# Kernel tuning notes

Hardware: AMD Instinct MI355X
Metric: run time of the kernel (lower is better)

The kernel has to match this reference:

```python
import jax, jax.numpy as jnp
import numpy as np

LN_EPS = 1e-5

def _ln(x, g, b):
    m = x.mean(-1, keepdims=True)
    v = ((x - m) ** 2).mean(-1, keepdims=True)
    return (x - m) * jax.lax.rsqrt(v + LN_EPS) * g + b

def setup_inputs() -> dict:
    key = jax.random.key(0)
    B, Q, K, H, NH, L = 4, 32, 8192, 1024, 16, 128
    ks = jax.random.split(key, 10)
    def p(k, shape):
        return jax.random.normal(k, shape, jnp.float32) * 0.02
    return {
        "question_emb": jax.random.normal(ks[0], (B, Q, H), jnp.float32),
        "context_emb": jax.random.normal(ks[1], (B, K, H), jnp.float32),
        "Wq_l": p(ks[2], (H, H)), "bq_l": jnp.zeros((H,), jnp.float32),
        "Wk_l": p(ks[3], (H, H)), "bk_l": jnp.zeros((H,), jnp.float32),
        "Wq_g": p(ks[4], (H, H)), "bq_g": jnp.zeros((H,), jnp.float32),
        "Wk_g": p(ks[5], (H, H)), "bk_g": jnp.zeros((H,), jnp.float32),
        "ln_g": jnp.ones((H,), jnp.float32), "ln_b": jnp.zeros((H,), jnp.float32),
        "gp_W1": p(ks[6], (2 * H, H)), "gp_b1": jnp.zeros((H,), jnp.float32),
        "gp_W2": p(ks[7], (H, 1)), "gp_b2": jnp.zeros((1,), jnp.float32),
        "num_heads": NH,
        "chunk_len": L,
    }

def reference(question_emb, context_emb, Wq_l, bq_l, Wk_l, bk_l,
              Wq_g, bq_g, Wk_g, bk_g, ln_g, ln_b,
              gp_W1, gp_b1, gp_W2, gp_b2, num_heads, chunk_len):
    B, Qn, H = question_emb.shape
    K = context_emb.shape[1]
    nh, L = num_heads, chunk_len
    d = H // nh
    J = K // L
    scale = 1.0 / np.sqrt(d)

    # ---- Global scorer: one cross-attn over all K, then per-chunk mean pooling ----
    qh = (question_emb @ Wq_g + bq_g).reshape(B, Qn, nh, d).transpose(0, 2, 1, 3)   # [B,nh,Q,d]
    kh = (context_emb @ Wk_g + bk_g).reshape(B, K, nh, d).transpose(0, 2, 1, 3)     # [B,nh,K,d]
    wg = jax.nn.softmax(jnp.einsum('bhqd,bhkd->bhqk', qh, kh) * scale, axis=-1)     # [B,nh,Q,K]
    attn = wg.mean(axis=(1, 2))                                                     # [B,K]
    global_scores = jax.nn.softmax(attn.reshape(B, J, L).mean(-1), axis=-1)         # [B,J]

    # ---- Local scorer: per-chunk cross-attn (batched over chunks), max-over-keys pooling ----
    qh_l = (question_emb @ Wq_l + bq_l).reshape(B, Qn, nh, d).transpose(0, 2, 1, 3)  # [B,nh,Q,d]
    kh_l = (context_emb @ Wk_l + bk_l).reshape(B, J, L, nh, d).transpose(0, 1, 3, 2, 4)  # [B,J,nh,L,d]
    s_l = jnp.einsum('bhqd,bjhld->bjhql', qh_l, kh_l) * scale                        # [B,J,nh,Q,L]
    w_l = jax.nn.softmax(s_l, axis=-1)
    local_scores = jax.nn.softmax(w_l.max(-1).mean(axis=(2, 3)), axis=-1)            # [B,J]

    # ---- Router: LN'd mean-pool vecs -> gate MLP -> fuse -> softmax ----
    q_vec = _ln(question_emb.mean(1), ln_g, ln_b)                                    # [B,H]
    c_vec = _ln(context_emb.reshape(B, J, L, H).mean(2), ln_g, ln_b)                 # [B,J,H]
    g_in = jnp.concatenate([jnp.broadcast_to(q_vec[:, None, :], (B, J, H)), c_vec], -1)
    h1 = jax.nn.gelu(g_in @ gp_W1 + gp_b1, approximate=False)
    gate = jax.nn.sigmoid(h1 @ gp_W2 + gp_b2)[..., 0]                                # [B,J]
    fused = gate * local_scores + (1.0 - gate) * global_scores
    final_scores = jax.nn.softmax(fused, axis=-1)                                    # [B,J]
    global_gate = final_scores.mean(-1).reshape(B, 1, 1)
    return final_scores, local_scores, global_scores, global_gate
```

## Files before the change

kernel.cpp:

```cpp
#include <hip/hip_runtime.h>
#include <math.h>

#define B_    4
#define QN    32
#define KN    8192
#define HDIM  1024
#define NHD   16
#define DH    64
#define LCH   128
#define JCH   64

typedef float f32x4 __attribute__((ext_vector_type(4)));
typedef short s16x8 __attribute__((ext_vector_type(8)));
typedef unsigned short u16;

__device__ __forceinline__ u16 f2bf(float f) {
  unsigned u = __float_as_uint(f);
  u += 0x7fffu + ((u >> 16) & 1u);
  return (u16)(u >> 16);
}

__device__ __forceinline__ void llds16(const void* g, void* l) {
  __builtin_amdgcn_global_load_lds((const __attribute__((address_space(1))) unsigned int*)g,
                                   (__attribute__((address_space(3))) unsigned int*)l,
                                   16, 0, 0);
}

__device__ __forceinline__ void gemm64_direct(const float* __restrict__ A, const float* __restrict__ Bm,
                                              float* __restrict__ C, int m0, int n0, char* smem) {
  float (*As)[17] = (float(*)[17])smem;
  float (*Bs)[64] = (float(*)[64])(smem + 4352);
  int t = threadIdx.x;
  int tm = t >> 4, tn = t & 15;
  int ra = t >> 2, ka = (t & 3) * 4;
  int kb = t >> 4, nb = (t & 15) * 4;
  float c[4][4];
#pragma unroll
  for (int i = 0; i < 4; ++i)
#pragma unroll
    for (int j = 0; j < 4; ++j) c[i][j] = 0.f;
  float4 va = *(const float4*)(A + (size_t)(m0 + ra) * HDIM + ka);
  float4 vb = *(const float4*)(Bm + (size_t)kb * HDIM + n0 + nb);
  for (int kk = 0; kk < HDIM; kk += 16) {
    As[ra][ka] = va.x; As[ra][ka + 1] = va.y; As[ra][ka + 2] = va.z; As[ra][ka + 3] = va.w;
    *(float4*)&Bs[kb][nb] = vb;
    __syncthreads();
    if (kk + 16 < HDIM) {
      va = *(const float4*)(A + (size_t)(m0 + ra) * HDIM + kk + 16 + ka);
      vb = *(const float4*)(Bm + (size_t)(kk + 16 + kb) * HDIM + n0 + nb);
    }
#pragma unroll
    for (int kq = 0; kq < 16; ++kq) {
      float a0 = As[tm * 4 + 0][kq], a1 = As[tm * 4 + 1][kq];
      float a2 = As[tm * 4 + 2][kq], a3 = As[tm * 4 + 3][kq];
      float b0 = Bs[kq][tn * 4 + 0], b1 = Bs[kq][tn * 4 + 1];
      float b2 = Bs[kq][tn * 4 + 2], b3 = Bs[kq][tn * 4 + 3];
      c[0][0] += a0 * b0; c[0][1] += a0 * b1; c[0][2] += a0 * b2; c[0][3] += a0 * b3;
      c[1][0] += a1 * b0; c[1][1] += a1 * b1; c[1][2] += a1 * b2; c[1][3] += a1 * b3;
      c[2][0] += a2 * b0; c[2][1] += a2 * b1; c[2][2] += a2 * b2; c[2][3] += a2 * b3;
      c[3][0] += a3 * b0; c[3][1] += a3 * b1; c[3][2] += a3 * b2; c[3][3] += a3 * b3;
    }
    __syncthreads();
  }
#pragma unroll
  for (int i = 0; i < 4; ++i)
#pragma unroll
    for (int j = 0; j < 4; ++j)
      C[(size_t)(m0 + tm * 4 + i) * HDIM + n0 + tn * 4 + j] = c[i][j];
}

__global__ __launch_bounds__(256) void k_cvt(const float* __restrict__ ctx, u16* __restrict__ ctxb,
                                             float* __restrict__ csum4,
                                             const float* __restrict__ question,
                                             const float* __restrict__ Wq_g, const float* __restrict__ Wq_l,
                                             float* __restrict__ qh,
                                             const float* __restrict__ g, const float* __restrict__ lb,
                                             float* __restrict__ qvec, float* __restrict__ qpart) {
  __shared__ __align__(16) char smem[8448];
  int blk = blockIdx.x, t = threadIdx.x;
  if (blk < 64) {
    int s2 = blk >> 5, mt = (blk >> 4) & 1, ntile = blk & 15;
    gemm64_direct(question, s2 ? Wq_l : Wq_g, qh + (size_t)s2 * 131072, mt * 64, ntile * 64, smem);
  } else if (blk < 68) {
    int b = blk - 64;
    const float* p = question + (size_t)b * QN * HDIM + t * 4;
    float a0 = 0, a1 = 0, a2 = 0, a3 = 0;
    for (int r = 0; r < QN; ++r) {
      float4 v = *(const float4*)(p + (size_t)r * HDIM);
      a0 += v.x; a1 += v.y; a2 += v.z; a3 += v.w;
    }
    const float sc = 1.0f / QN;
    a0 *= sc; a1 *= sc; a2 *= sc; a3 *= sc;
    float s = a0 + a1 + a2 + a3;
    float ss = a0 * a0 + a1 * a1 + a2 * a2 + a3 * a3;
#pragma unroll
    for (int o = 1; o < 64; o <<= 1) { s += __shfl_xor(s, o, 64); ss += __shfl_xor(ss, o, 64); }
    float* sm = (float*)smem; float* sq = sm + 4;
    int wid = t >> 6, lane = t & 63;
    if (lane == 0) { sm[wid] = s; sq[wid] = ss; }
    __syncthreads();
    float S = sm[0] + sm[1] + sm[2] + sm[3], SS = sq[0] + sq[1] + sq[2] + sq[3];
    float mu = S / HDIM;
    float inv = rsqrtf(SS / HDIM - mu * mu + 1e-5f);
    int c = t * 4;
    float4 o;
    o.x = (a0 - mu) * inv * g[c + 0] + lb[c + 0];
    o.y = (a1 - mu) * inv * g[c + 1] + lb[c + 1];
    o.z = (a2 - mu) * inv * g[c + 2] + lb[c + 2];
    o.w = (a3 - mu) * inv * g[c + 3] + lb[c + 3];
    *(float4*)&qvec[(size_t)b * HDIM + c] = o;
  } else if (blk == 68) {
    float4 z = make_float4(0.f, 0.f, 0.f, 0.f);
#pragma unroll
    for (int i = 0; i < 4; ++i) ((float4*)qpart)[t * 4 + i] = z;
  } else {
    int cb = blk - 69;
    int bj = cb >> 2, seg = cb & 3;
    const float* p = ctx + ((size_t)bj * LCH + seg * 32) * HDIM + t * 4;
    u16* op = ctxb + ((size_t)bj * LCH + seg * 32) * HDIM + t * 4;
    float a0 = 0, a1 = 0, a2 = 0, a3 = 0;
    for (int r0 = 0; r0 < 32; r0 += 8) {
      float4 v[8];
#pragma unroll
      for (int r = 0; r < 8; ++r) v[r] = *(const float4*)(p + (size_t)(r0 + r) * HDIM);
#pragma unroll
      for (int r = 0; r < 8; ++r) {
        ushort4 o;
        o.x = f2bf(v[r].x); o.y = f2bf(v[r].y); o.z = f2bf(v[r].z); o.w = f2bf(v[r].w);
        *(ushort4*)(op + (size_t)(r0 + r) * HDIM) = o;
        a0 += v[r].x; a1 += v[r].y; a2 += v[r].z; a3 += v[r].w;
      }
    }
    *(float4*)&csum4[((size_t)bj * 4 + seg) * HDIM + t * 4] = make_float4(a0, a1, a2, a3);
  }
}

__global__ __launch_bounds__(256) void k_mid(const float* __restrict__ qh,
                                             const float* __restrict__ Wk_g, const float* __restrict__ Wk_l,
                                             const float* __restrict__ bq_g, const float* __restrict__ bq_l,
                                             u16* __restrict__ Ab,
                                             const float* __restrict__ bk_g, const float* __restrict__ bk_l,
                                             float* __restrict__ sbias,
                                             const float* __restrict__ qvec, const float* __restrict__ W1,
                                             float* __restrict__ qpart,
                                             const float* __restrict__ csum4,
                                             const float* __restrict__ g, const float* __restrict__ lb,
                                             float* __restrict__ cvec) {
  __shared__ __align__(16) char smem[8448];
  int blk = blockIdx.x, t = threadIdx.x;
  if (blk < 512) {
    int ct = blk & 3, slot = (blk >> 2) & 31, b = blk >> 7;
    int s2 = slot >> 4, h = slot & 15;
    const float* qhp = qh + (size_t)(s2 * 4 + b) * QN * HDIM;
    const float* Wk = s2 ? Wk_l : Wk_g;
    const float* bq = s2 ? bq_l : bq_g;
    float (*qs)[DH] = (float(*)[DH])smem;
    {
      int q = t >> 3, doff = (t & 7) * 8;
      const float4* src = (const float4*)(qhp + (size_t)q * HDIM + h * DH + doff);
      float4 b0 = *(const float4*)(bq + h * DH + doff);
      float4 b1 = *(const float4*)(bq + h * DH + doff + 4);
      float4 v0 = src[0], v1 = src[1];
      qs[q][doff + 0] = v0.x + b0.x; qs[q][doff + 1] = v0.y + b0.y;
      qs[q][doff + 2] = v0.z + b0.z; qs[q][doff + 3] = v0.w + b0.w;
      qs[q][doff + 4] = v1.x + b1.x; qs[q][doff + 5] = v1.y + b1.y;
      qs[q][doff + 6] = v1.z + b1.z; qs[q][doff + 7] = v1.w + b1.w;
    }
    __syncthreads();
    int c = ct * 256 + t;
    float w[DH];
    const float* wr = Wk + (size_t)c * HDIM + h * DH;
#pragma unroll
    for (int d = 0; d < DH; d += 4) {
      float4 v = *(const float4*)(wr + d);
      w[d] = v.x; w[d + 1] = v.y; w[d + 2] = v.z; w[d + 3] = v.w;
    }
    u16* outp = Ab + ((size_t)b * HDIM + s2 * 512 + h * QN) * HDIM + c;
    for (int q = 0; q < QN; ++q) {
      float acc = 0.f;
#pragma unroll
      for (int d = 0; d < DH; ++d) acc += qs[q][d] * w[d];
      outp[(size_t)q * HDIM] = f2bf(acc * 0.125f);
    }
  } else if (blk < 768) {
    int id = blk - 512;
    int nt = id & 3, b = (id >> 2) & 3, ks = id >> 4;
    int n = nt * 256 + t;
    const float* qv = qvec + (size_t)b * HDIM + ks * 64;
    const float* wp = W1 + (size_t)ks * 64 * HDIM + n;
    float acc = 0.f;
#pragma unroll 8
    for (int c = 0; c < 64; ++c) acc += qv[c] * wp[(size_t)c * HDIM];
    atomicAdd(&qpart[(size_t)b * HDIM + n], acc);
  } else if (blk < 1024) {
    int bj = blk - 768;
    const float* cs = csum4 + (size_t)bj * 4 * HDIM + t * 4;
    float4 v0 = *(const float4*)(cs);
    float4 v1 = *(const float4*)(cs + HDIM);
    float4 v2 = *(const float4*)(cs + 2 * HDIM);
    float4 v3 = *(const float4*)(cs + 3 * HDIM);
    const float sc = 1.0f / LCH;
    float a0 = (v0.x + v1.x + v2.x + v3.x) * sc;
    float a1 = (v0.y + v1.y + v2.y + v3.y) * sc;
    float a2 = (v0.z + v1.z + v2.z + v3.z) * sc;
    float a3 = (v0.w + v1.w + v2.w + v3.w) * sc;
    float s = a0 + a1 + a2 + a3;
    float ss = a0 * a0 + a1 * a1 + a2 * a2 + a3 * a3;
#pragma unroll
    for (int o = 1; o < 64; o <<= 1) { s += __shfl_xor(s, o, 64); ss += __shfl_xor(ss, o, 64); }
    float* sm = (float*)smem; float* sq = sm + 4;
    int wid = t >> 6, lane = t & 63;
    if (lane == 0) { sm[wid] = s; sq[wid] = ss; }
    __syncthreads();
    float S = sm[0] + sm[1] + sm[2] + sm[3], SS = sq[0] + sq[1] + sq[2] + sq[3];
    float mu = S / HDIM;
    float inv = rsqrtf(SS / HDIM - mu * mu + 1e-5f);
    int c = t * 4;
    float4 o;
    o.x = (a0 - mu) * inv * g[c + 0] + lb[c + 0];
    o.y = (a1 - mu) * inv * g[c + 1] + lb[c + 1];
    o.z = (a2 - mu) * inv * g[c + 2] + lb[c + 2];
    o.w = (a3 - mu) * inv * g[c + 3] + lb[c + 3];
    *(float4*)&cvec[(size_t)bj * HDIM + c] = o;
  } else {
    int i = (blk - 1024) * 256 + t;
    int b = i >> 10, n = i & (HDIM - 1);
    int s2 = n >> 9, hq = n & 511, h = hq >> 5, q = hq & 31;
    const float* qr = qh + ((size_t)(s2 * 4 + b) * QN + q) * HDIM + h * DH;
    const float* bk = (s2 ? bk_l : bk_g) + h * DH;
    const float* bq = (s2 ? bq_l : bq_g) + h * DH;
    float acc = 0.f;
#pragma unroll
    for (int d = 0; d < DH; ++d) acc += (qr[d] + bq[d]) * bk[d];
    sbias[i] = acc * 0.125f;
  }
}

__global__ __launch_bounds__(512, 2) void k_scores(const u16* __restrict__ ctxb, const u16* __restrict__ Ab,
                                                   const float* __restrict__ sbias,
                                                   float* __restrict__ mglob, float* __restrict__ zglob,
                                                   float* __restrict__ locinv) {
  __shared__ u16 lds[65536];
  u16* A0 = lds;           u16* B0 = lds + 16384;
  u16* A1 = lds + 32768;   u16* B1 = lds + 49152;
  int bid = blockIdx.x;
  int work = (bid & 7) * 64 + (bid >> 3);
  int b = work >> 7, rem = work & 127, rt = rem >> 2, nt = rem & 3;
  int t = threadIdx.x, wid = t >> 6, lane = t & 63;
  int wm = wid >> 2, wn = wid & 3;
  int lrow = lane & 15, lkg = lane >> 4;

  const u16* ctx0 = ctxb + ((size_t)b * KN + rt * 256) * HDIM;
  const u16* Afp  = Ab + ((size_t)b * HDIM + nt * 256) * HDIM;

  int grow = wid * 8 + (lane >> 3);
  int gslot = (lane & 7) ^ (lane >> 3);
  const u16* gA[4]; const u16* gB[4]; int dof[4];
#pragma unroll
  for (int s = 0; s < 4; ++s) {
    gA[s] = ctx0 + (size_t)(s * 64 + grow) * HDIM + gslot * 8;
    gB[s] = Afp + (size_t)(s * 64 + grow) * HDIM + gslot * 8;
    dof[s] = s * 4096 + wid * 512;
  }

  int rowA = (wm * 128 + lrow) * 64;
  int rowB = (wn * 64 + lrow) * 64;
  int p8[2];
#pragma unroll
  for (int ks = 0; ks < 2; ++ks) p8[ks] = ((ks * 4 + lkg) ^ (lane & 7)) * 8;

  f32x4 acc[8][4];
#pragma unroll
  for (int mi = 0; mi < 8; ++mi)
#pragma unroll
    for (int ni = 0; ni < 4; ++ni) acc[mi][ni] = 0.f;

#define STAGE(AT, BT, KT) { \
  _Pragma("unroll") for (int s = 0; s < 4; ++s) { \
    llds16(gA[s] + (KT) * 64, (AT) + dof[s]); \
    llds16(gB[s] + (KT) * 64, (BT) + dof[s]); } }

#define COMPUTE(AT, BT) { \
  _Pragma("unroll") for (int ks = 0; ks < 2; ++ks) { \
    const u16* pA = (AT) + rowA + p8[ks]; \
    const u16* pB = (BT) + rowB + p8[ks]; \
    s16x8 av[8], bv[4]; \
    _Pragma("unroll") for (int mi = 0; mi < 8; ++mi) av[mi] = *(const s16x8*)(pA + mi * 1024); \
    _Pragma("unroll") for (int ni = 0; ni < 4; ++ni) bv[ni] = *(const s16x8*)(pB + ni * 1024); \
    _Pragma("unroll") for (int mi = 0; mi < 8; ++mi) \
    _Pragma("unroll") for (int ni = 0; ni < 4; ++ni) \
      acc[mi][ni] = __builtin_amdgcn_mfma_f32_16x16x32_bf16(av[mi], bv[ni], acc[mi][ni], 0, 0, 0); } }

#define SYNCN(N) { asm volatile("s_waitcnt vmcnt(" #N ")" ::: "memory"); \
                   __builtin_amdgcn_s_barrier(); \
                   __builtin_amdgcn_sched_barrier(0); }

#define SUB(KT, CA, CB, SA, SB, FULL) { \
  if (FULL) { STAGE(SA, SB, (KT) + 1); } \
  if (FULL) { SYNCN(8) } else { SYNCN(0) } \
  __builtin_amdgcn_s_setprio(1); \
  COMPUTE(CA, CB); \
  __builtin_amdgcn_s_setprio(0); \
  __builtin_amdgcn_s_barrier(); }

  STAGE(A0, B0, 0);
  SUB(0,  A0, B0, A1, B1, 1)
  SUB(1,  A1, B1, A0, B0, 1)
  SUB(2,  A0, B0, A1, B1, 1)
  SUB(3,  A1, B1, A0, B0, 1)
  SUB(4,  A0, B0, A1, B1, 1)
  SUB(5,  A1, B1, A0, B0, 1)
  SUB(6,  A0, B0, A1, B1, 1)
  SUB(7,  A1, B1, A0, B0, 1)
  SUB(8,  A0, B0, A1, B1, 1)
  SUB(9,  A1, B1, A0, B0, 1)
  SUB(10, A0, B0, A1, B1, 1)
  SUB(11, A1, B1, A0, B0, 1)
  SUB(12, A0, B0, A1, B1, 1)
  SUB(13, A1, B1, A0, B0, 1)
  SUB(14, A0, B0, A1, B1, 1)
  SUB(15, A1, B1, A0, B0, 0)
#undef STAGE
#undef COMPUTE
#undef SYNCN
#undef SUB

  int jc = rt * 2 + wm;
  float sb[4];
#pragma unroll
  for (int ni = 0; ni < 4; ++ni)
    sb[ni] = sbias[b * HDIM + nt * 256 + wn * 64 + ni * 16 + lrow];
#pragma unroll
  for (int ni = 0; ni < 4; ++ni) {
    float m = -1e30f;
#pragma unroll
    for (int mi = 0; mi < 8; ++mi)
#pragma unroll
      for (int r = 0; r < 4; ++r) m = fmaxf(m, acc[mi][ni][r]);
    m += sb[ni];
    m = fmaxf(m, __shfl_xor(m, 16, 64));
    m = fmaxf(m, __shfl_xor(m, 32, 64));
    float z = 0.f;
#pragma unroll
    for (int mi = 0; mi < 8; ++mi)
#pragma unroll
      for (int r = 0; r < 4; ++r) z += __expf(acc[mi][ni][r] + sb[ni] - m);
    z += __shfl_xor(z, 16, 64);
    z += __shfl_xor(z, 32, 64);
    if (lane < 16) {
      int n = nt * 256 + wn * 64 + ni * 16 + lane;
      if (n < 512) {
        size_t o = ((size_t)b * 512 + n) * JCH + jc;
        mglob[o] = m; zglob[o] = z;
      } else {
        locinv[((size_t)b * JCH + jc) * 512 + (n - 512)] = 1.0f / z;
      }
    }
  }
}

__global__ __launch_bounds__(256) void k_post(const float* __restrict__ cvec, const float* __restrict__ W1,
                                              float* __restrict__ h1,
                                              const float* __restrict__ mglob, const float* __restrict__ zglob,
                                              float* __restrict__ Mh, float* __restrict__ Zr) {
  __shared__ __align__(16) char smem[8448];
  int blk = blockIdx.x, t = threadIdx.x;
  if (blk < 64) {
    int mt = blk >> 4, ntile = blk & 15;
    gemm64_direct(cvec, W1 + 1048576, h1, mt * 64, ntile * 64, smem);
  } else {
    int id = (blk - 64) * 256 + t;
    int b = id >> 9, hq = id & 511;
    const float* mg = mglob + ((size_t)b * 512 + hq) * JCH;
    const float* zg = zglob + ((size_t)b * 512 + hq) * JCH;
    float m = -1e30f;
    for (int j = 0; j < JCH; ++j) m = fmaxf(m, mg[j]);
    float z = 0.f;
    for (int j = 0; j < JCH; ++j) z += zg[j] * __expf(mg[j] - m);
    Mh[id] = m;
    Zr[id] = 1.0f / z;
  }
}

__global__ __launch_bounds__(256) void k_chunk(const float* __restrict__ mglob, const float* __restrict__ zglob,
                                               const float* __restrict__ locinv,
                                               const float* __restrict__ Mh, const float* __restrict__ Zr,
                                               const float* __restrict__ h1, const float* __restrict__ qpart,
                                               const float* __restrict__ b1, const float* __restrict__ W2,
                                               float* __restrict__ abuf, float* __restrict__ lbuf,
                                               float* __restrict__ gbuf) {
  int bj = blockIdx.x, t = threadIdx.x;
  int b = bj >> 6, j = bj & 63;
  const float* mg = mglob + (size_t)b * 512 * JCH + j;
  const float* zg = zglob + (size_t)b * 512 * JCH + j;
  const float* lp = locinv + (size_t)bj * 512;
  const float* Mb = Mh + (size_t)b * 512;
  const float* Zb = Zr + (size_t)b * 512;
  float a = 0.f, l = 0.f, gsum = 0.f;
  for (int hq = t; hq < 512; hq += 256) {
    a += zg[(size_t)hq * JCH] * __expf(mg[(size_t)hq * JCH] - Mb[hq]) * Zb[hq];
    l += lp[hq];
  }
  const float* hp = h1 + (size_t)bj * HDIM;
  const float* qp = qpart + (size_t)b * HDIM;
  for (int n = t; n < HDIM; n += 256) {
    float x = hp[n] + qp[n] + b1[n];
    x = x * 0.5f * (1.0f + erff(x * 0.70710678118654752f));
    gsum += x * W2[n];
  }
#pragma unroll
  for (int o = 1; o < 64; o <<= 1) {
    a += __shfl_xor(a, o, 64); l += __shfl_xor(l, o, 64); gsum += __shfl_xor(gsum, o, 64);
  }
  __shared__ float ra[4], rl[4], rg[4];
  int wid = t >> 6, lane = t & 63;
  if (lane == 0) { ra[wid] = a; rl[wid] = l; rg[wid] = gsum; }
  __syncthreads();
  if (t == 0) {
    abuf[bj] = (ra[0] + ra[1] + ra[2] + ra[3]) * (1.0f / 65536.0f);
    lbuf[bj] = (rl[0] + rl[1] + rl[2] + rl[3]) * (1.0f / 512.0f);
    gbuf[bj] = rg[0] + rg[1] + rg[2] + rg[3];
  }
}

__global__ __launch_bounds__(64) void k_final(const float* __restrict__ abuf, const float* __restrict__ lbuf,
                                              const float* __restrict__ gbuf, const float* __restrict__ b2,
                                              float* __restrict__ out) {
  int b = blockIdx.x, t = threadIdx.x;
  float a = abuf[b * 64 + t];
  float l = lbuf[b * 64 + t];
  float gt = gbuf[b * 64 + t] + b2[0];
  gt = 1.0f / (1.0f + __expf(-gt));
  float am = a, lm = l;
#pragma unroll
  for (int o = 1; o < 64; o <<= 1) { am = fmaxf(am, __shfl_xor(am, o, 64)); lm = fmaxf(lm, __shfl_xor(lm, o, 64)); }
  float ae = __expf(a - am), le = __expf(l - lm);
  float as_ = ae, ls_ = le;
#pragma unroll
  for (int o = 1; o < 64; o <<= 1) { as_ += __shfl_xor(as_, o, 64); ls_ += __shfl_xor(ls_, o, 64); }
  float gs = ae / as_, ls = le / ls_;
  float fu = gt * ls + (1.0f - gt) * gs;
  float fm = fu;
#pragma unroll
  for (int o = 1; o < 64; o <<= 1) fm = fmaxf(fm, __shfl_xor(fm, o, 64));
  float fe = __expf(fu - fm);
  float fs_ = fe;
#pragma unroll
  for (int o = 1; o < 64; o <<= 1) fs_ += __shfl_xor(fs_, o, 64);
  float fv = fe / fs_;
  out[b * 64 + t] = fv;
  out[256 + b * 64 + t] = ls;
  out[512 + b * 64 + t] = gs;
  float tot = fv;
#pragma unroll
  for (int o = 1; o < 64; o <<= 1) tot += __shfl_xor(tot, o, 64);
  if (t == 0) out[768 + b] = tot * (1.0f / 64.0f);
}

extern "C" void kernel_launch(void* const* d_in, const int* in_sizes, int n_in,
                              void* d_out, int out_size, void* d_ws, size_t ws_size,
                              hipStream_t stream) {
  const float* question = (const float*)d_in[0];
  const float* context  = (const float*)d_in[1];
  const float* Wq_l = (const float*)d_in[2];
  const float* bq_l = (const float*)d_in[3];
  const float* Wk_l = (const float*)d_in[4];
  const float* bk_l = (const float*)d_in[5];
  const float* Wq_g = (const float*)d_in[6];
  const float* bq_g = (const float*)d_in[7];
  const float* Wk_g = (const float*)d_in[8];
  const float* bk_g = (const float*)d_in[9];
  const float* ln_g = (const float*)d_in[10];
  const float* ln_b = (const float*)d_in[11];
  const float* W1   = (const float*)d_in[12];
  const float* b1   = (const float*)d_in[13];
  const float* W2   = (const float*)d_in[14];
  const float* b2   = (const float*)d_in[15];

  char* ws = (char*)d_ws;
  u16*   ctxb   = (u16*)(ws + 0);
  u16*   Ab     = (u16*)(ws + 67108864);
  float* qh     = (float*)(ws + 75497472);
  float* sbias  = (float*)(ws + 76546048);
  float* mglob  = (float*)(ws + 76562432);
  float* zglob  = (float*)(ws + 77086720);
  float* locinv = (float*)(ws + 77611008);
  float* qvec   = (float*)(ws + 78135296);
  float* cvec   = (float*)(ws + 78151680);
  float* qpart  = (float*)(ws + 79200256);
  float* h1     = (float*)(ws + 79216640);
  float* Mh     = (float*)(ws + 80265216);
  float* Zr     = (float*)(ws + 80273408);
  float* abuf   = (float*)(ws + 80281600);
  float* lbuf   = (float*)(ws + 80282624);
  float* gbuf   = (float*)(ws + 80283648);
  float* csum4  = (float*)(ws + 80284672);

  hipLaunchKernelGGL(k_cvt, dim3(1093), dim3(256), 0, stream,
                     context, ctxb, csum4, question, Wq_g, Wq_l, qh, ln_g, ln_b, qvec, qpart);
  hipLaunchKernelGGL(k_mid, dim3(1040), dim3(256), 0, stream,
                     qh, Wk_g, Wk_l, bq_g, bq_l, Ab, bk_g, bk_l, sbias, qvec, W1, qpart,
                     csum4, ln_g, ln_b, cvec);
  hipLaunchKernelGGL(k_scores, dim3(512), dim3(512), 0, stream, ctxb, Ab, sbias, mglob, zglob, locinv);
  hipLaunchKernelGGL(k_post, dim3(72), dim3(256), 0, stream, cvec, W1, h1, mglob, zglob, Mh, Zr);
  hipLaunchKernelGGL(k_chunk, dim3(256), dim3(256), 0, stream, mglob, zglob, locinv, Mh, Zr, h1, qpart, b1, W2, abuf, lbuf, gbuf);
  hipLaunchKernelGGL(k_final, dim3(4), dim3(64), 0, stream, abuf, lbuf, gbuf, b2, (float*)d_out);
}
```

Measured before the change: 198.8 us.

## Split context conversion from chunk sums and move LayerNorm into scores kernel

The first kernel now does only a flat grid-stride fp32-to-bf16 conversion of the context across 2048 blocks. It no longer computes per-chunk column sums at the same time. Those sums are recomputed in the second kernel by reading back the bf16 copy, and the chunk LayerNorm moves into extra blocks appended to the scores kernel. The aim is a more uniform, bandwidth-friendly conversion and some overlap of small work with the big scores GEMM. The cost is an extra read of the 64 MB bf16 context and chunk means taken from bf16-rounded values, a small change in precision.

```diff
diff --git a/kernel.cpp b/kernel.cpp
--- a/kernel.cpp
+++ b/kernel.cpp
@@ -18,6 +18,10 @@
   unsigned u = __float_as_uint(f);
   u += 0x7fffu + ((u >> 16) & 1u);
   return (u16)(u >> 16);
+}
+
+__device__ __forceinline__ float bf2f(u16 v) {
+  return __uint_as_float(((unsigned)v) << 16);
 }
 
 __device__ __forceinline__ void llds16(const void* g, void* l) {
@@ -69,13 +73,12 @@
       C[(size_t)(m0 + tm * 4 + i) * HDIM + n0 + tn * 4 + j] = c[i][j];
 }
 
-__global__ __launch_bounds__(256) void k_cvt(const float* __restrict__ ctx, u16* __restrict__ ctxb,
-                                             float* __restrict__ csum4,
-                                             const float* __restrict__ question,
-                                             const float* __restrict__ Wq_g, const float* __restrict__ Wq_l,
-                                             float* __restrict__ qh,
-                                             const float* __restrict__ g, const float* __restrict__ lb,
-                                             float* __restrict__ qvec, float* __restrict__ qpart) {
+__global__ __launch_bounds__(256) void k_go(const float* __restrict__ ctx, u16* __restrict__ ctxb,
+                                            const float* __restrict__ question,
+                                            const float* __restrict__ Wq_g, const float* __restrict__ Wq_l,
+                                            float* __restrict__ qh,
+                                            const float* __restrict__ g, const float* __restrict__ lb,
+                                            float* __restrict__ qvec, float* __restrict__ qpart) {
   __shared__ __align__(16) char smem[8448];
   int blk = blockIdx.x, t = threadIdx.x;
   if (blk < 64) {
@@ -114,24 +117,14 @@
 #pragma unroll
     for (int i = 0; i < 4; ++i) ((float4*)qpart)[t * 4 + i] = z;
   } else {
-    int cb = blk - 69;
-    int bj = cb >> 2, seg = cb & 3;
-    const float* p = ctx + ((size_t)bj * LCH + seg * 32) * HDIM + t * 4;
-    u16* op = ctxb + ((size_t)bj * LCH + seg * 32) * HDIM + t * 4;
-    float a0 = 0, a1 = 0, a2 = 0, a3 = 0;
-    for (int r0 = 0; r0 < 32; r0 += 8) {
-      float4 v[8];
-#pragma unroll
-      for (int r = 0; r < 8; ++r) v[r] = *(const float4*)(p + (size_t)(r0 + r) * HDIM);
-#pragma unroll
-      for (int r = 0; r < 8; ++r) {
-        ushort4 o;
-        o.x = f2bf(v[r].x); o.y = f2bf(v[r].y); o.z = f2bf(v[r].z); o.w = f2bf(v[r].w);
-        *(ushort4*)(op + (size_t)(r0 + r) * HDIM) = o;
-        a0 += v[r].x; a1 += v[r].y; a2 += v[r].z; a3 += v[r].w;
-      }
-    }
-    *(float4*)&csum4[((size_t)bj * 4 + seg) * HDIM + t * 4] = make_float4(a0, a1, a2, a3);
+    const int total4 = B_ * KN * HDIM / 4;
+    int idx = (blk - 69) * 256 + t;
+    for (int i = idx; i < total4; i += 2048 * 256) {
+      float4 v = ((const float4*)ctx)[i];
+      ushort4 o;
+      o.x = f2bf(v.x); o.y = f2bf(v.y); o.z = f2bf(v.z); o.w = f2bf(v.w);
+      ((ushort4*)ctxb)[i] = o;
+    }
   }
 }
 
@@ -143,9 +136,7 @@
                                              float* __restrict__ sbias,
                                              const float* __restrict__ qvec, const float* __restrict__ W1,
                                              float* __restrict__ qpart,
-                                             const float* __restrict__ csum4,
-                                             const float* __restrict__ g, const float* __restrict__ lb,
-                                             float* __restrict__ cvec) {
+                                             const u16* __restrict__ ctxb, float* __restrict__ csum4) {
   __shared__ __align__(16) char smem[8448];
   int blk = blockIdx.x, t = threadIdx.x;
   if (blk < 512) {
@@ -182,8 +173,18 @@
       for (int d = 0; d < DH; ++d) acc += qs[q][d] * w[d];
       outp[(size_t)q * HDIM] = f2bf(acc * 0.125f);
     }
-  } else if (blk < 768) {
-    int id = blk - 512;
+  } else if (blk < 1536) {
+    int cb = blk - 512;
+    int bj = cb >> 2, seg = cb & 3;
+    const u16* p = ctxb + ((size_t)bj * LCH + seg * 32) * HDIM + t * 4;
+    float a0 = 0, a1 = 0, a2 = 0, a3 = 0;
+    for (int r = 0; r < 32; ++r) {
+      ushort4 v = *(const ushort4*)(p + (size_t)r * HDIM);
+      a0 += bf2f(v.x); a1 += bf2f(v.y); a2 += bf2f(v.z); a3 += bf2f(v.w);
+    }
+    *(float4*)&csum4[((size_t)bj * 4 + seg) * HDIM + t * 4] = make_float4(a0, a1, a2, a3);
+  } else if (blk < 1792) {
+    int id = blk - 1536;
     int nt = id & 3, b = (id >> 2) & 3, ks = id >> 4;
     int n = nt * 256 + t;
     const float* qv = qvec + (size_t)b * HDIM + ks * 64;
@@ -192,9 +193,34 @@
 #pragma unroll 8
     for (int c = 0; c < 64; ++c) acc += qv[c] * wp[(size_t)c * HDIM];
     atomicAdd(&qpart[(size_t)b * HDIM + n], acc);
-  } else if (blk < 1024) {
-    int bj = blk - 768;
-    const float* cs = csum4 + (size_t)bj * 4 * HDIM + t * 4;
+  } else {
+    int i = (blk - 1792) * 256 + t;
+    int b = i >> 10, n = i & (HDIM - 1);
+    int s2 = n >> 9, hq = n & 511, h = hq >> 5, q = hq & 31;
+    const float* qr = qh + ((size_t)(s2 * 4 + b) * QN + q) * HDIM + h * DH;
+    const float* bk = (s2 ? bk_l : bk_g) + h * DH;
+    const float* bq = (s2 ? bq_l : bq_g) + h * DH;
+    float acc = 0.f;
+#pragma unroll
+    for (int d = 0; d < DH; ++d) acc += (qr[d] + bq[d]) * bk[d];
+    sbias[i] = acc * 0.125f;
+  }
+}
+
+__global__ __launch_bounds__(512, 2) void k_scores(const u16* __restrict__ ctxb, const u16* __restrict__ Ab,
+                                                   const float* __restrict__ sbias,
+                                                   float* __restrict__ mglob, float* __restrict__ zglob,
+                                                   float* __restrict__ locinv,
+                                                   const float* __restrict__ csum4,
+                                                   const float* __restrict__ g, const float* __restrict__ lb,
+                                                   float* __restrict__ cvec) {
+  __shared__ u16 lds[65536];
+  int bid = blockIdx.x;
+  int t = threadIdx.x;
+  if (bid >= 512) {
+    int rb = bid - 512, half = t >> 8, tt = t & 255;
+    int bj = rb * 2 + half;
+    const float* cs = csum4 + (size_t)bj * 4 * HDIM + tt * 4;
     float4 v0 = *(const float4*)(cs);
     float4 v1 = *(const float4*)(cs + HDIM);
     float4 v2 = *(const float4*)(cs + 2 * HDIM);
@@ -208,45 +234,28 @@
     float ss = a0 * a0 + a1 * a1 + a2 * a2 + a3 * a3;
 #pragma unroll
     for (int o = 1; o < 64; o <<= 1) { s += __shfl_xor(s, o, 64); ss += __shfl_xor(ss, o, 64); }
-    float* sm = (float*)smem; float* sq = sm + 4;
+    float* smf = (float*)lds;
     int wid = t >> 6, lane = t & 63;
-    if (lane == 0) { sm[wid] = s; sq[wid] = ss; }
+    if (lane == 0) { smf[wid] = s; smf[8 + wid] = ss; }
     __syncthreads();
-    float S = sm[0] + sm[1] + sm[2] + sm[3], SS = sq[0] + sq[1] + sq[2] + sq[3];
+    float S = smf[half * 4 + 0] + smf[half * 4 + 1] + smf[half * 4 + 2] + smf[half * 4 + 3];
+    float SS = smf[8 + half * 4 + 0] + smf[8 + half * 4 + 1] + smf[8 + half * 4 + 2] + smf[8 + half * 4 + 3];
     float mu = S / HDIM;
     float inv = rsqrtf(SS / HDIM - mu * mu + 1e-5f);
-    int c = t * 4;
+    int c = tt * 4;
     float4 o;
     o.x = (a0 - mu) * inv * g[c + 0] + lb[c + 0];
     o.y = (a1 - mu) * inv * g[c + 1] + lb[c + 1];
     o.z = (a2 - mu) * inv * g[c + 2] + lb[c + 2];
     o.w = (a3 - mu) * inv * g[c + 3] + lb[c + 3];
     *(float4*)&cvec[(size_t)bj * HDIM + c] = o;
-  } else {
-    int i = (blk - 1024) * 256 + t;
-    int b = i >> 10, n = i & (HDIM - 1);
-    int s2 = n >> 9, hq = n & 511, h = hq >> 5, q = hq & 31;
-    const float* qr = qh + ((size_t)(s2 * 4 + b) * QN + q) * HDIM + h * DH;
-    const float* bk = (s2 ? bk_l : bk_g) + h * DH;
-    const float* bq = (s2 ? bq_l : bq_g) + h * DH;
-    float acc = 0.f;
-#pragma unroll
-    for (int d = 0; d < DH; ++d) acc += (qr[d] + bq[d]) * bk[d];
-    sbias[i] = acc * 0.125f;
-  }
-}
-
-__global__ __launch_bounds__(512, 2) void k_scores(const u16* __restrict__ ctxb, const u16* __restrict__ Ab,
-                                                   const float* __restrict__ sbias,
-                                                   float* __restrict__ mglob, float* __restrict__ zglob,
-                                                   float* __restrict__ locinv) {
-  __shared__ u16 lds[65536];
+    return;
+  }
   u16* A0 = lds;           u16* B0 = lds + 16384;
   u16* A1 = lds + 32768;   u16* B1 = lds + 49152;
-  int bid = blockIdx.x;
   int work = (bid & 7) * 64 + (bid >> 3);
   int b = work >> 7, rem = work & 127, rt = rem >> 2, nt = rem & 3;
-  int t = threadIdx.x, wid = t >> 6, lane = t & 63;
+  int wid = t >> 6, lane = t & 63;
   int wm = wid >> 2, wn = wid & 3;
   int lrow = lane & 15, lkg = lane >> 4;
 
@@ -496,12 +505,13 @@
   float* gbuf   = (float*)(ws + 80283648);
   float* csum4  = (float*)(ws + 80284672);
 
-  hipLaunchKernelGGL(k_cvt, dim3(1093), dim3(256), 0, stream,
-                     context, ctxb, csum4, question, Wq_g, Wq_l, qh, ln_g, ln_b, qvec, qpart);
-  hipLaunchKernelGGL(k_mid, dim3(1040), dim3(256), 0, stream,
+  hipLaunchKernelGGL(k_go, dim3(2117), dim3(256), 0, stream,
+                     context, ctxb, question, Wq_g, Wq_l, qh, ln_g, ln_b, qvec, qpart);
+  hipLaunchKernelGGL(k_mid, dim3(1808), dim3(256), 0, stream,
                      qh, Wk_g, Wk_l, bq_g, bq_l, Ab, bk_g, bk_l, sbias, qvec, W1, qpart,
+                     ctxb, csum4);
+  hipLaunchKernelGGL(k_scores, dim3(640), dim3(512), 0, stream, ctxb, Ab, sbias, mglob, zglob, locinv,
                      csum4, ln_g, ln_b, cvec);
-  hipLaunchKernelGGL(k_scores, dim3(512), dim3(512), 0, stream, ctxb, Ab, sbias, mglob, zglob, locinv);
   hipLaunchKernelGGL(k_post, dim3(72), dim3(256), 0, stream, cvec, W1, h1, mglob, zglob, Mh, Zr);
   hipLaunchKernelGGL(k_chunk, dim3(256), dim3(256), 0, stream, mglob, zglob, locinv, Mh, Zr, h1, qpart, b1, W2, abuf, lbuf, gbuf);
   hipLaunchKernelGGL(k_final, dim3(4), dim3(64), 0, stream, abuf, lbuf, gbuf, b2, (float*)d_out);
```

Measured after the change: 199.4 us. No clear change (+0.3%).

## Fuse fp32-to-bf16 context conversion into the scores GEMM A-operand load

Applied to the files above, without the earlier changes.

Removes the bf16 copy of the context that the first kernel wrote and the scores kernel reread. The scores kernel now loads fp32 context rows into registers, converts them to bf16 and writes them into swizzled LDS, interleaving the conversion with the two MFMA k-substeps. This saves the intermediate write and its reread, but the GEMM now fetches twice the bytes per A tile and drops the asynchronous direct-to-LDS path for A, so it waits with full vmcnt(0) barriers. The bias blocks in the mid kernel are also reordered ahead of the chunk layer-norm blocks.

```diff
diff --git a/kernel.cpp b/kernel.cpp
--- a/kernel.cpp
+++ b/kernel.cpp
@@ -69,13 +69,12 @@
       C[(size_t)(m0 + tm * 4 + i) * HDIM + n0 + tn * 4 + j] = c[i][j];
 }
 
-__global__ __launch_bounds__(256) void k_cvt(const float* __restrict__ ctx, u16* __restrict__ ctxb,
-                                             float* __restrict__ csum4,
-                                             const float* __restrict__ question,
-                                             const float* __restrict__ Wq_g, const float* __restrict__ Wq_l,
-                                             float* __restrict__ qh,
-                                             const float* __restrict__ g, const float* __restrict__ lb,
-                                             float* __restrict__ qvec, float* __restrict__ qpart) {
+__global__ __launch_bounds__(256) void k_go(const float* __restrict__ ctx, float* __restrict__ csum4,
+                                            const float* __restrict__ question,
+                                            const float* __restrict__ Wq_g, const float* __restrict__ Wq_l,
+                                            float* __restrict__ qh,
+                                            const float* __restrict__ g, const float* __restrict__ lb,
+                                            float* __restrict__ qvec, float* __restrict__ qpart) {
   __shared__ __align__(16) char smem[8448];
   int blk = blockIdx.x, t = threadIdx.x;
   if (blk < 64) {
@@ -117,19 +116,11 @@
     int cb = blk - 69;
     int bj = cb >> 2, seg = cb & 3;
     const float* p = ctx + ((size_t)bj * LCH + seg * 32) * HDIM + t * 4;
-    u16* op = ctxb + ((size_t)bj * LCH + seg * 32) * HDIM + t * 4;
     float a0 = 0, a1 = 0, a2 = 0, a3 = 0;
-    for (int r0 = 0; r0 < 32; r0 += 8) {
-      float4 v[8];
-#pragma unroll
-      for (int r = 0; r < 8; ++r) v[r] = *(const float4*)(p + (size_t)(r0 + r) * HDIM);
-#pragma unroll
-      for (int r = 0; r < 8; ++r) {
-        ushort4 o;
-        o.x = f2bf(v[r].x); o.y = f2bf(v[r].y); o.z = f2bf(v[r].z); o.w = f2bf(v[r].w);
-        *(ushort4*)(op + (size_t)(r0 + r) * HDIM) = o;
-        a0 += v[r].x; a1 += v[r].y; a2 += v[r].z; a3 += v[r].w;
-      }
+#pragma unroll 4
+    for (int r = 0; r < 32; ++r) {
+      float4 v = *(const float4*)(p + (size_t)r * HDIM);
+      a0 += v.x; a1 += v.y; a2 += v.z; a3 += v.w;
     }
     *(float4*)&csum4[((size_t)bj * 4 + seg) * HDIM + t * 4] = make_float4(a0, a1, a2, a3);
   }
@@ -192,8 +183,19 @@
 #pragma unroll 8
     for (int c = 0; c < 64; ++c) acc += qv[c] * wp[(size_t)c * HDIM];
     atomicAdd(&qpart[(size_t)b * HDIM + n], acc);
-  } else if (blk < 1024) {
-    int bj = blk - 768;
+  } else if (blk < 784) {
+    int i = (blk - 768) * 256 + t;
+    int b = i >> 10, n = i & (HDIM - 1);
+    int s2 = n >> 9, hq = n & 511, h = hq >> 5, q = hq & 31;
+    const float* qr = qh + ((size_t)(s2 * 4 + b) * QN + q) * HDIM + h * DH;
+    const float* bk = (s2 ? bk_l : bk_g) + h * DH;
+    const float* bq = (s2 ? bq_l : bq_g) + h * DH;
+    float acc = 0.f;
+#pragma unroll
+    for (int d = 0; d < DH; ++d) acc += (qr[d] + bq[d]) * bk[d];
+    sbias[i] = acc * 0.125f;
+  } else {
+    int bj = blk - 784;
     const float* cs = csum4 + (size_t)bj * 4 * HDIM + t * 4;
     float4 v0 = *(const float4*)(cs);
     float4 v1 = *(const float4*)(cs + HDIM);
@@ -222,21 +224,10 @@
     o.z = (a2 - mu) * inv * g[c + 2] + lb[c + 2];
     o.w = (a3 - mu) * inv * g[c + 3] + lb[c + 3];
     *(float4*)&cvec[(size_t)bj * HDIM + c] = o;
-  } else {
-    int i = (blk - 1024) * 256 + t;
-    int b = i >> 10, n = i & (HDIM - 1);
-    int s2 = n >> 9, hq = n & 511, h = hq >> 5, q = hq & 31;
-    const float* qr = qh + ((size_t)(s2 * 4 + b) * QN + q) * HDIM + h * DH;
-    const float* bk = (s2 ? bk_l : bk_g) + h * DH;
-    const float* bq = (s2 ? bq_l : bq_g) + h * DH;
-    float acc = 0.f;
-#pragma unroll
-    for (int d = 0; d < DH; ++d) acc += (qr[d] + bq[d]) * bk[d];
-    sbias[i] = acc * 0.125f;
-  }
-}
-
-__global__ __launch_bounds__(512, 2) void k_scores(const u16* __restrict__ ctxb, const u16* __restrict__ Ab,
+  }
+}
+
+__global__ __launch_bounds__(512, 2) void k_scores(const float* __restrict__ ctx, const u16* __restrict__ Ab,
                                                    const float* __restrict__ sbias,
                                                    float* __restrict__ mglob, float* __restrict__ zglob,
                                                    float* __restrict__ locinv) {
@@ -250,17 +241,22 @@
   int wm = wid >> 2, wn = wid & 3;
   int lrow = lane & 15, lkg = lane >> 4;
 
-  const u16* ctx0 = ctxb + ((size_t)b * KN + rt * 256) * HDIM;
-  const u16* Afp  = Ab + ((size_t)b * HDIM + nt * 256) * HDIM;
+  const u16* Afp = Ab + ((size_t)b * HDIM + nt * 256) * HDIM;
+
+  int arow = t >> 1, ahalf = t & 1;
+  const float* ga = ctx + ((size_t)b * KN + rt * 256 + arow) * HDIM + ahalf * 32;
+  int awoff[4];
+#pragma unroll
+  for (int jj = 0; jj < 4; ++jj)
+    awoff[jj] = arow * 64 + ((ahalf * 4 + jj) ^ (arow & 7)) * 8;
 
   int grow = wid * 8 + (lane >> 3);
   int gslot = (lane & 7) ^ (lane >> 3);
-  const u16* gA[4]; const u16* gB[4]; int dof[4];
+  const u16* gB[4]; int dofB[4];
 #pragma unroll
   for (int s = 0; s < 4; ++s) {
-    gA[s] = ctx0 + (size_t)(s * 64 + grow) * HDIM + gslot * 8;
     gB[s] = Afp + (size_t)(s * 64 + grow) * HDIM + gslot * 8;
-    dof[s] = s * 4096 + wid * 512;
+    dofB[s] = s * 4096 + wid * 512;
   }
 
   int rowA = (wm * 128 + lrow) * 64;
@@ -275,35 +271,56 @@
 #pragma unroll
     for (int ni = 0; ni < 4; ++ni) acc[mi][ni] = 0.f;
 
-#define STAGE(AT, BT, KT) { \
-  _Pragma("unroll") for (int s = 0; s < 4; ++s) { \
-    llds16(gA[s] + (KT) * 64, (AT) + dof[s]); \
-    llds16(gB[s] + (KT) * 64, (BT) + dof[s]); } }
-
-#define COMPUTE(AT, BT) { \
-  _Pragma("unroll") for (int ks = 0; ks < 2; ++ks) { \
-    const u16* pA = (AT) + rowA + p8[ks]; \
-    const u16* pB = (BT) + rowB + p8[ks]; \
-    s16x8 av[8], bv[4]; \
-    _Pragma("unroll") for (int mi = 0; mi < 8; ++mi) av[mi] = *(const s16x8*)(pA + mi * 1024); \
-    _Pragma("unroll") for (int ni = 0; ni < 4; ++ni) bv[ni] = *(const s16x8*)(pB + ni * 1024); \
-    _Pragma("unroll") for (int mi = 0; mi < 8; ++mi) \
-    _Pragma("unroll") for (int ni = 0; ni < 4; ++ni) \
-      acc[mi][ni] = __builtin_amdgcn_mfma_f32_16x16x32_bf16(av[mi], bv[ni], acc[mi][ni], 0, 0, 0); } }
-
-#define SYNCN(N) { asm volatile("s_waitcnt vmcnt(" #N ")" ::: "memory"); \
-                   __builtin_amdgcn_s_barrier(); \
-                   __builtin_amdgcn_sched_barrier(0); }
+#define LOADA(F, KT) { \
+  _Pragma("unroll") for (int q = 0; q < 8; ++q) \
+    F[q] = *(const float4*)(ga + (size_t)(KT) * 64 + q * 4); }
+
+#define CVT2(AT, F, J0) { \
+  _Pragma("unroll") for (int jj = (J0); jj < (J0) + 2; ++jj) { \
+    float4 x = F[2 * jj], y = F[2 * jj + 1]; \
+    s16x8 o; \
+    o[0] = (short)f2bf(x.x); o[1] = (short)f2bf(x.y); o[2] = (short)f2bf(x.z); o[3] = (short)f2bf(x.w); \
+    o[4] = (short)f2bf(y.x); o[5] = (short)f2bf(y.y); o[6] = (short)f2bf(y.z); o[7] = (short)f2bf(y.w); \
+    *(s16x8*)((AT) + awoff[jj]) = o; } }
+
+#define STAGEB(BT, KT) { \
+  _Pragma("unroll") for (int s = 0; s < 4; ++s) \
+    llds16(gB[s] + (KT) * 64, (BT) + dofB[s]); }
+
+#define COMPUTE_KS(AT, BT, ks) { \
+  const u16* pA = (AT) + rowA + p8[ks]; \
+  const u16* pB = (BT) + rowB + p8[ks]; \
+  s16x8 av[8], bv[4]; \
+  _Pragma("unroll") for (int mi = 0; mi < 8; ++mi) av[mi] = *(const s16x8*)(pA + mi * 1024); \
+  _Pragma("unroll") for (int ni = 0; ni < 4; ++ni) bv[ni] = *(const s16x8*)(pB + ni * 1024); \
+  _Pragma("unroll") for (int mi = 0; mi < 8; ++mi) \
+  _Pragma("unroll") for (int ni = 0; ni < 4; ++ni) \
+    acc[mi][ni] = __builtin_amdgcn_mfma_f32_16x16x32_bf16(av[mi], bv[ni], acc[mi][ni], 0, 0, 0); }
+
+#define BARRIER() { asm volatile("s_waitcnt vmcnt(0) lgkmcnt(0)" ::: "memory"); \
+                    __builtin_amdgcn_s_barrier(); \
+                    __builtin_amdgcn_sched_barrier(0); }
 
 #define SUB(KT, CA, CB, SA, SB, FULL) { \
-  if (FULL) { STAGE(SA, SB, (KT) + 1); } \
-  if (FULL) { SYNCN(8) } else { SYNCN(0) } \
+  float4 F[8]; \
+  if (FULL) { LOADA(F, (KT) + 1); STAGEB(SB, (KT) + 1); } \
   __builtin_amdgcn_s_setprio(1); \
-  COMPUTE(CA, CB); \
+  COMPUTE_KS(CA, CB, 0); \
   __builtin_amdgcn_s_setprio(0); \
-  __builtin_amdgcn_s_barrier(); }
-
-  STAGE(A0, B0, 0);
+  if (FULL) { CVT2(SA, F, 0); } \
+  __builtin_amdgcn_s_setprio(1); \
+  COMPUTE_KS(CA, CB, 1); \
+  __builtin_amdgcn_s_setprio(0); \
+  if (FULL) { CVT2(SA, F, 2); BARRIER(); } }
+
+  {
+    float4 F[8];
+    LOADA(F, 0);
+    STAGEB(B0, 0);
+    CVT2(A0, F, 0);
+    CVT2(A0, F, 2);
+  }
+  BARRIER();
   SUB(0,  A0, B0, A1, B1, 1)
   SUB(1,  A1, B1, A0, B0, 1)
   SUB(2,  A0, B0, A1, B1, 1)
@@ -320,9 +337,11 @@
   SUB(13, A1, B1, A0, B0, 1)
   SUB(14, A0, B0, A1, B1, 1)
   SUB(15, A1, B1, A0, B0, 0)
-#undef STAGE
-#undef COMPUTE
-#undef SYNCN
+#undef LOADA
+#undef CVT2
+#undef STAGEB
+#undef COMPUTE_KS
+#undef BARRIER
 #undef SUB
 
   int jc = rt * 2 + wm;
@@ -478,7 +497,6 @@
   const float* b2   = (const float*)d_in[15];
 
   char* ws = (char*)d_ws;
-  u16*   ctxb   = (u16*)(ws + 0);
   u16*   Ab     = (u16*)(ws + 67108864);
   float* qh     = (float*)(ws + 75497472);
   float* sbias  = (float*)(ws + 76546048);
@@ -496,12 +514,12 @@
   float* gbuf   = (float*)(ws + 80283648);
   float* csum4  = (float*)(ws + 80284672);
 
-  hipLaunchKernelGGL(k_cvt, dim3(1093), dim3(256), 0, stream,
-                     context, ctxb, csum4, question, Wq_g, Wq_l, qh, ln_g, ln_b, qvec, qpart);
+  hipLaunchKernelGGL(k_go, dim3(1093), dim3(256), 0, stream,
+                     context, csum4, question, Wq_g, Wq_l, qh, ln_g, ln_b, qvec, qpart);
   hipLaunchKernelGGL(k_mid, dim3(1040), dim3(256), 0, stream,
                      qh, Wk_g, Wk_l, bq_g, bq_l, Ab, bk_g, bk_l, sbias, qvec, W1, qpart,
                      csum4, ln_g, ln_b, cvec);
-  hipLaunchKernelGGL(k_scores, dim3(512), dim3(512), 0, stream, ctxb, Ab, sbias, mglob, zglob, locinv);
+  hipLaunchKernelGGL(k_scores, dim3(512), dim3(512), 0, stream, context, Ab, sbias, mglob, zglob, locinv);
   hipLaunchKernelGGL(k_post, dim3(72), dim3(256), 0, stream, cvec, W1, h1, mglob, zglob, Mh, Zr);
   hipLaunchKernelGGL(k_chunk, dim3(256), dim3(256), 0, stream, mglob, zglob, locinv, Mh, Zr, h1, qpart, b1, W2, abuf, lbuf, gbuf);
   hipLaunchKernelGGL(k_final, dim3(4), dim3(64), 0, stream, abuf, lbuf, gbuf, b2, (float*)d_out);
```

Result: slower. 251.2 us (+26.3%).
